# Kernel tuning notes

Hardware: AMD Instinct MI355X
Metric: run time of the kernel (lower is better)

Reference implementation:

```python
import jax, jax.numpy as jnp
import numpy as np

N = 4096
IN_DIM = 128
OUT_DIM = 64
LEAKY_SLOPE = 0.2


def setup_inputs() -> dict:
    key = jax.random.key(0)
    ks = jax.random.split(key, 8)
    H = jax.random.normal(ks[0], (N, IN_DIM), dtype=jnp.float32)
    # dense 0/1 adjacency per relation (int constants w.r.t. autodiff)
    A_buys = jax.random.randint(ks[1], (N, N), 0, 2, dtype=jnp.int32)
    A_views = jax.random.randint(ks[2], (N, N), 0, 2, dtype=jnp.int32)
    # xavier_uniform for W (stored [in, out]; Wh = H @ W == torch Linear with weight W.T)
    s_w = float(np.sqrt(6.0 / (IN_DIM + OUT_DIM)))
    W_buys = jax.random.uniform(ks[3], (IN_DIM, OUT_DIM), jnp.float32, -s_w, s_w)
    W_views = jax.random.uniform(ks[4], (IN_DIM, OUT_DIM), jnp.float32, -s_w, s_w)
    # xavier_uniform on a.view(1, 2*out_dim)
    s_a = float(np.sqrt(6.0 / (1 + 2 * OUT_DIM)))
    a_buys = jax.random.uniform(ks[5], (2 * OUT_DIM,), jnp.float32, -s_a, s_a)
    a_views = jax.random.uniform(ks[6], (2 * OUT_DIM,), jnp.float32, -s_a, s_a)
    bias = jnp.zeros((OUT_DIM,), dtype=jnp.float32)
    return {"H": H, "A_buys": A_buys, "A_views": A_views,
            "W_buys": W_buys, "W_views": W_views,
            "a_buys": a_buys, "a_views": a_views, "bias": bias}


def _relation(H, A, W, a):
    Wh = H @ W                                  # [N, OUT]
    # (cat(Wh_i, Wh_j) * a).sum(-1) == Wh_i @ a[:OUT] + Wh_j @ a[OUT:]
    s_i = Wh @ a[:OUT_DIM]                      # [N]
    s_j = Wh @ a[OUT_DIM:]                      # [N]
    e = jax.nn.leaky_relu(s_i[:, None] + s_j[None, :], LEAKY_SLOPE)  # [N, N]
    e = jnp.where(A == 0, -jnp.inf, e)
    alpha = jnp.nan_to_num(jax.nn.softmax(e, axis=1))                # isolated rows -> 0
    return alpha @ Wh                           # [N, OUT]


def reference(H, A_buys, A_views, W_buys, W_views, a_buys, a_views, bias):
    agg = _relation(H, A_buys, W_buys, a_buys) + _relation(H, A_views, W_views, a_views)
    return agg + bias
```

## Files before the change

kernel.cpp:

```cpp
#include <hip/hip_runtime.h>

#define NN 4096
#define IND 128
#define OUTD 64
#define NSPLIT 2

typedef __attribute__((ext_vector_type(4))) float  floatx4;
typedef __attribute__((ext_vector_type(8))) __bf16 bf16x8;
typedef __attribute__((ext_vector_type(4))) int    intx4;

__device__ __forceinline__ unsigned short f2bf(float f) {
  unsigned int u = __float_as_uint(f);
  u += 0x7fffu + ((u >> 16) & 1u);
  return (unsigned short)(u >> 16);
}

__device__ __forceinline__ float wcalc(int a, float s) {
  float l = s > 0.f ? s : 0.2f * s;
  float e = __expf(l);
  return a != 0 ? e : 0.f;
}

__global__ __launch_bounds__(256) void gat_prep(
    const float* __restrict__ H,
    const float* __restrict__ W0, const float* __restrict__ W1,
    const float* __restrict__ av0, const float* __restrict__ av1,
    unsigned short* __restrict__ whT,
    float* __restrict__ sA,
    float* __restrict__ sB)
{
  const int rel = blockIdx.y;
  const float* __restrict__ W  = rel ? W1 : W0;
  const float* __restrict__ av = rel ? av1 : av0;
  const int i0 = blockIdx.x * 16;
  const int t = threadIdx.x;
  const int c = t & 63;
  const int wv = __builtin_amdgcn_readfirstlane(t >> 6);
  const float* __restrict__ hp = H + (size_t)(i0 + wv * 4) * IND;

  float acc0 = 0.f, acc1 = 0.f, acc2 = 0.f, acc3 = 0.f;
#pragma unroll 8
  for (int k = 0; k < IND; k += 4) {
    float4 h0 = *(const float4*)(hp + k);
    float4 h1 = *(const float4*)(hp + IND + k);
    float4 h2 = *(const float4*)(hp + 2 * IND + k);
    float4 h3 = *(const float4*)(hp + 3 * IND + k);
    float w0 = W[(k + 0) * OUTD + c];
    float w1 = W[(k + 1) * OUTD + c];
    float w2 = W[(k + 2) * OUTD + c];
    float w3 = W[(k + 3) * OUTD + c];
    acc0 += h0.x * w0 + h0.y * w1 + h0.z * w2 + h0.w * w3;
    acc1 += h1.x * w0 + h1.y * w1 + h1.z * w2 + h1.w * w3;
    acc2 += h2.x * w0 + h2.y * w1 + h2.z * w2 + h2.w * w3;
    acc3 += h3.x * w0 + h3.y * w1 + h3.z * w2 + h3.w * w3;
  }

  const float alo = av[c], ahi = av[OUTD + c];
  float pa0 = acc0 * alo, pa1 = acc1 * alo, pa2 = acc2 * alo, pa3 = acc3 * alo;
  float pb0 = acc0 * ahi, pb1 = acc1 * ahi, pb2 = acc2 * ahi, pb3 = acc3 * ahi;
#pragma unroll
  for (int off = 32; off >= 1; off >>= 1) {
    pa0 += __shfl_xor(pa0, off); pa1 += __shfl_xor(pa1, off);
    pa2 += __shfl_xor(pa2, off); pa3 += __shfl_xor(pa3, off);
    pb0 += __shfl_xor(pb0, off); pb1 += __shfl_xor(pb1, off);
    pb2 += __shfl_xor(pb2, off); pb3 += __shfl_xor(pb3, off);
  }
  const int ibase = i0 + wv * 4;
  if (c == 0) {
    float* sa = sA + rel * NN + ibase;
    float* sb = sB + rel * NN + ibase;
    sa[0] = pa0; sa[1] = pa1; sa[2] = pa2; sa[3] = pa3;
    sb[0] = pb0; sb[1] = pb1; sb[2] = pb2; sb[3] = pb3;
  }

  unsigned long long packed =
      (unsigned long long)f2bf(acc0)        | ((unsigned long long)f2bf(acc1) << 16) |
      ((unsigned long long)f2bf(acc2) << 32) | ((unsigned long long)f2bf(acc3) << 48);
  *(unsigned long long*)(whT + (size_t)(rel * OUTD + c) * NN + ibase) = packed;
}

__global__ __launch_bounds__(512) void gat_main(
    const int* __restrict__ A0, const int* __restrict__ A1,
    const unsigned short* __restrict__ whT,
    const float* __restrict__ sA, const float* __restrict__ sB,
    float* __restrict__ numer,
    float* __restrict__ denom)
{
  __shared__ float red[8][1024];
  __shared__ float dred[8][16];
  const int rel  = blockIdx.y;
  const int sp   = blockIdx.z;
  const int i0   = blockIdx.x * 16;
  const int t    = threadIdx.x;
  const int w    = t >> 6;
  const int lane = t & 63;
  const int m    = lane & 15;
  const int quad = lane >> 4;
  const int i    = i0 + m;
  const int* __restrict__ A = rel ? A1 : A0;
  const float si = sA[rel * NN + i];
  const float* __restrict__ sb = sB + rel * NN;
  const unsigned short* __restrict__ wh = whT + (size_t)rel * OUTD * NN;

  const int jbase = sp * (NN / NSPLIT) + w * 256 + quad * 8;
  const int*            pA  = A  + (size_t)i * NN + jbase;
  const float*          psb = sb + jbase;
  const unsigned short* pb0 = wh + (size_t)(0 * 16 + m) * NN + jbase;
  const unsigned short* pb1 = wh + (size_t)(1 * 16 + m) * NN + jbase;
  const unsigned short* pb2 = wh + (size_t)(2 * 16 + m) * NN + jbase;
  const unsigned short* pb3 = wh + (size_t)(3 * 16 + m) * NN + jbase;

  floatx4 acc0 = {0.f, 0.f, 0.f, 0.f}, acc1 = acc0, acc2 = acc0, acc3 = acc0;
  float dsum = 0.f;

#pragma unroll 2
  for (int jt = 0; jt < 256; jt += 32) {
    intx4 a0 = __builtin_nontemporal_load((const intx4*)(pA + jt));
    intx4 a1 = __builtin_nontemporal_load((const intx4*)(pA + jt + 4));
    float4 s0 = *(const float4*)(psb + jt);
    float4 s1 = *(const float4*)(psb + jt + 4);
    bf16x8 b0 = *(const bf16x8*)(pb0 + jt);
    bf16x8 b1 = *(const bf16x8*)(pb1 + jt);
    bf16x8 b2 = *(const bf16x8*)(pb2 + jt);
    bf16x8 b3 = *(const bf16x8*)(pb3 + jt);

    float e0 = wcalc(a0[0], si + s0.x);
    float e1 = wcalc(a0[1], si + s0.y);
    float e2 = wcalc(a0[2], si + s0.z);
    float e3 = wcalc(a0[3], si + s0.w);
    float e4 = wcalc(a1[0], si + s1.x);
    float e5 = wcalc(a1[1], si + s1.y);
    float e6 = wcalc(a1[2], si + s1.z);
    float e7 = wcalc(a1[3], si + s1.w);
    dsum += ((e0 + e1) + (e2 + e3)) + ((e4 + e5) + (e6 + e7));

    bf16x8 af;
    af[0] = (__bf16)e0; af[1] = (__bf16)e1; af[2] = (__bf16)e2; af[3] = (__bf16)e3;
    af[4] = (__bf16)e4; af[5] = (__bf16)e5; af[6] = (__bf16)e6; af[7] = (__bf16)e7;

    acc0 = __builtin_amdgcn_mfma_f32_16x16x32_bf16(af, b0, acc0, 0, 0, 0);
    acc1 = __builtin_amdgcn_mfma_f32_16x16x32_bf16(af, b1, acc1, 0, 0, 0);
    acc2 = __builtin_amdgcn_mfma_f32_16x16x32_bf16(af, b2, acc2, 0, 0, 0);
    acc3 = __builtin_amdgcn_mfma_f32_16x16x32_bf16(af, b3, acc3, 0, 0, 0);
  }

  dsum += __shfl_xor(dsum, 16);
  dsum += __shfl_xor(dsum, 32);

#pragma unroll
  for (int r = 0; r < 4; r++) {
    const int row = quad * 4 + r;
    red[w][row * 64 + 0 * 16 + m] = acc0[r];
    red[w][row * 64 + 1 * 16 + m] = acc1[r];
    red[w][row * 64 + 2 * 16 + m] = acc2[r];
    red[w][row * 64 + 3 * 16 + m] = acc3[r];
  }
  if (lane < 16) dred[w][lane] = dsum;
  __syncthreads();

  const int c  = t & 63;
  const int r0 = t >> 6;
  const size_t base = ((size_t)rel * NSPLIT + sp) * NN;
#pragma unroll
  for (int rr = r0; rr < 16; rr += 8) {
    float ns = 0.f, ds = 0.f;
#pragma unroll
    for (int ww = 0; ww < 8; ww++) { ns += red[ww][rr * 64 + c]; ds += dred[ww][rr]; }
    numer[(base + i0 + rr) * OUTD + c] = ns;
    if (c == 0) denom[base + i0 + rr] = ds;
  }
}

__global__ __launch_bounds__(256) void gat_combine(
    const float* __restrict__ numer, const float* __restrict__ denom,
    const float* __restrict__ bias, float* __restrict__ out)
{
  const int idx = blockIdx.x * 256 + threadIdx.x;
  const int i  = idx >> 4;
  const int c4 = idx & 15;
  const float4* nv = (const float4*)numer;

  float4 o = ((const float4*)bias)[c4];
#pragma unroll
  for (int rel = 0; rel < 2; rel++) {
    float4 n = {0.f, 0.f, 0.f, 0.f};
    float  d = 0.f;
#pragma unroll
    for (int s = 0; s < NSPLIT; s++) {
      const size_t base = ((size_t)rel * NSPLIT + s) * NN + i;
      float4 np = nv[base * 16 + c4];
      n.x += np.x; n.y += np.y; n.z += np.z; n.w += np.w;
      d += denom[base];
    }
    float inv = d > 0.f ? 1.f / d : 0.f;
    o.x += n.x * inv; o.y += n.y * inv; o.z += n.z * inv; o.w += n.w * inv;
  }
  ((float4*)out)[idx] = o;
}

extern "C" void kernel_launch(void* const* d_in, const int* in_sizes, int n_in,
                              void* d_out, int out_size, void* d_ws, size_t ws_size,
                              hipStream_t stream) {
  const float* H    = (const float*)d_in[0];
  const int*   A0   = (const int*)d_in[1];
  const int*   A1   = (const int*)d_in[2];
  const float* W0   = (const float*)d_in[3];
  const float* W1   = (const float*)d_in[4];
  const float* av0  = (const float*)d_in[5];
  const float* av1  = (const float*)d_in[6];
  const float* bias = (const float*)d_in[7];
  float* out = (float*)d_out;

  unsigned short* whT = (unsigned short*)d_ws;
  float* sA    = (float*)((char*)d_ws + 2u * OUTD * NN * 2u);
  float* sB    = sA + 2 * NN;
  float* numer = sB + 2 * NN;
  float* denom = numer + (size_t)2 * NSPLIT * NN * OUTD;

  gat_prep<<<dim3(NN / 16, 2), 256, 0, stream>>>(H, W0, W1, av0, av1, whT, sA, sB);
  gat_main<<<dim3(NN / 16, 2, NSPLIT), 512, 0, stream>>>(A0, A1, whT, sA, sB, numer, denom);
  gat_combine<<<(NN * OUTD / 4) / 256, 256, 0, stream>>>(numer, denom, bias, out);
}
```

Before: 209.3 us.

## Pack adjacency into bitmasks in a separate pass before the attention kernel

A new gat_pack kernel uses wave ballots to compress both int32 adjacency matrices into 64-bit bitmasks. The main kernel then reads those bits instead of int32 values, which cuts the adjacency traffic it has to stream. The exponent is folded to exp2 with log2(e) pre-multiplied into the attention vectors, and leaky-relu becomes an fmax. The split count is now chosen at runtime from the workspace size. The full int32 adjacency is still read once by the pack pass, which adds a kernel launch and a bitmask write/read round trip.

```diff
diff --git a/kernel.cpp b/kernel.cpp
--- a/kernel.cpp
+++ b/kernel.cpp
@@ -3,11 +3,17 @@
 #define NN 4096
 #define IND 128
 #define OUTD 64
-#define NSPLIT 2
+#define LOG2E 1.44269504088896340736f
 
 typedef __attribute__((ext_vector_type(4))) float  floatx4;
 typedef __attribute__((ext_vector_type(8))) __bf16 bf16x8;
-typedef __attribute__((ext_vector_type(4))) int    intx4;
+typedef __attribute__((ext_vector_type(2))) unsigned long long u64x2;
+
+#if __has_builtin(__builtin_amdgcn_exp2f)
+#define EXP2(x) __builtin_amdgcn_exp2f(x)
+#else
+#define EXP2(x) exp2f(x)
+#endif
 
 __device__ __forceinline__ unsigned short f2bf(float f) {
   unsigned int u = __float_as_uint(f);
@@ -15,10 +21,32 @@
   return (unsigned short)(u >> 16);
 }
 
-__device__ __forceinline__ float wcalc(int a, float s) {
-  float l = s > 0.f ? s : 0.2f * s;
-  float e = __expf(l);
-  return a != 0 ? e : 0.f;
+__global__ __launch_bounds__(256) void gat_pack(
+    const int* __restrict__ A0, const int* __restrict__ A1,
+    unsigned long long* __restrict__ bits)
+{
+  const int t    = threadIdx.x;
+  const int lane = t & 63;
+  const int wv   = t >> 6;
+  const int unit = blockIdx.x * 4 + wv;
+  const int q    = unit & 3;
+  const int i    = (unit >> 2) & (NN - 1);
+  const int rel  = unit >> 14;
+  const int* __restrict__ A = (rel ? A1 : A0) + (size_t)i * NN + q * 1024 + lane;
+
+  unsigned long long wbuf[16];
+#pragma unroll
+  for (int k = 0; k < 16; k++)
+    wbuf[k] = __ballot(A[k * 64] != 0);
+
+  if (lane == 0) {
+    u64x2* dst = (u64x2*)(bits + ((size_t)rel * NN + i) * 64 + q * 16);
+#pragma unroll
+    for (int k = 0; k < 8; k++) {
+      u64x2 v; v[0] = wbuf[2 * k]; v[1] = wbuf[2 * k + 1];
+      dst[k] = v;
+    }
+  }
 }
 
 __global__ __launch_bounds__(256) void gat_prep(
@@ -55,7 +83,7 @@
     acc3 += h3.x * w0 + h3.y * w1 + h3.z * w2 + h3.w * w3;
   }
 
-  const float alo = av[c], ahi = av[OUTD + c];
+  const float alo = av[c] * LOG2E, ahi = av[OUTD + c] * LOG2E;
   float pa0 = acc0 * alo, pa1 = acc1 * alo, pa2 = acc2 * alo, pa3 = acc3 * alo;
   float pb0 = acc0 * ahi, pb1 = acc1 * ahi, pb2 = acc2 * ahi, pb3 = acc3 * ahi;
 #pragma unroll
@@ -80,11 +108,12 @@
 }
 
 __global__ __launch_bounds__(512) void gat_main(
-    const int* __restrict__ A0, const int* __restrict__ A1,
+    const unsigned long long* __restrict__ bits,
     const unsigned short* __restrict__ whT,
     const float* __restrict__ sA, const float* __restrict__ sB,
     float* __restrict__ numer,
-    float* __restrict__ denom)
+    float* __restrict__ denom,
+    int ns)
 {
   __shared__ float red[8][1024];
   __shared__ float dred[8][16];
@@ -97,51 +126,70 @@
   const int m    = lane & 15;
   const int quad = lane >> 4;
   const int i    = i0 + m;
-  const int* __restrict__ A = rel ? A1 : A0;
   const float si = sA[rel * NN + i];
   const float* __restrict__ sb = sB + rel * NN;
   const unsigned short* __restrict__ wh = whT + (size_t)rel * OUTD * NN;
-
-  const int jbase = sp * (NN / NSPLIT) + w * 256 + quad * 8;
-  const int*            pA  = A  + (size_t)i * NN + jbase;
-  const float*          psb = sb + jbase;
-  const unsigned short* pb0 = wh + (size_t)(0 * 16 + m) * NN + jbase;
-  const unsigned short* pb1 = wh + (size_t)(1 * 16 + m) * NN + jbase;
-  const unsigned short* pb2 = wh + (size_t)(2 * 16 + m) * NN + jbase;
-  const unsigned short* pb3 = wh + (size_t)(3 * 16 + m) * NN + jbase;
+  const unsigned long long* __restrict__ bp = bits + ((size_t)rel * NN + i) * 64;
+
+  const int jwin = NN / (ns * 8);
+  const int jw0  = sp * (NN / ns) + w * jwin;
+  const int nch  = jwin >> 8;
 
   floatx4 acc0 = {0.f, 0.f, 0.f, 0.f}, acc1 = acc0, acc2 = acc0, acc3 = acc0;
   float dsum = 0.f;
 
-#pragma unroll 2
-  for (int jt = 0; jt < 256; jt += 32) {
-    intx4 a0 = __builtin_nontemporal_load((const intx4*)(pA + jt));
-    intx4 a1 = __builtin_nontemporal_load((const intx4*)(pA + jt + 4));
-    float4 s0 = *(const float4*)(psb + jt);
-    float4 s1 = *(const float4*)(psb + jt + 4);
-    bf16x8 b0 = *(const bf16x8*)(pb0 + jt);
-    bf16x8 b1 = *(const bf16x8*)(pb1 + jt);
-    bf16x8 b2 = *(const bf16x8*)(pb2 + jt);
-    bf16x8 b3 = *(const bf16x8*)(pb3 + jt);
-
-    float e0 = wcalc(a0[0], si + s0.x);
-    float e1 = wcalc(a0[1], si + s0.y);
-    float e2 = wcalc(a0[2], si + s0.z);
-    float e3 = wcalc(a0[3], si + s0.w);
-    float e4 = wcalc(a1[0], si + s1.x);
-    float e5 = wcalc(a1[1], si + s1.y);
-    float e6 = wcalc(a1[2], si + s1.z);
-    float e7 = wcalc(a1[3], si + s1.w);
-    dsum += ((e0 + e1) + (e2 + e3)) + ((e4 + e5) + (e6 + e7));
-
-    bf16x8 af;
-    af[0] = (__bf16)e0; af[1] = (__bf16)e1; af[2] = (__bf16)e2; af[3] = (__bf16)e3;
-    af[4] = (__bf16)e4; af[5] = (__bf16)e5; af[6] = (__bf16)e6; af[7] = (__bf16)e7;
-
-    acc0 = __builtin_amdgcn_mfma_f32_16x16x32_bf16(af, b0, acc0, 0, 0, 0);
-    acc1 = __builtin_amdgcn_mfma_f32_16x16x32_bf16(af, b1, acc1, 0, 0, 0);
-    acc2 = __builtin_amdgcn_mfma_f32_16x16x32_bf16(af, b2, acc2, 0, 0, 0);
-    acc3 = __builtin_amdgcn_mfma_f32_16x16x32_bf16(af, b3, acc3, 0, 0, 0);
+  for (int c2 = 0; c2 < nch; c2++) {
+    const int jc = jw0 + c2 * 256;
+    u64x2 bA = *(const u64x2*)(bp + (jc >> 6));
+    u64x2 bB = *(const u64x2*)(bp + (jc >> 6) + 2);
+    const float*          psb = sb + jc + quad * 8;
+    const unsigned short* pb0 = wh + (size_t)(0 * 16 + m) * NN + jc + quad * 8;
+    const unsigned short* pb1 = wh + (size_t)(1 * 16 + m) * NN + jc + quad * 8;
+    const unsigned short* pb2 = wh + (size_t)(2 * 16 + m) * NN + jc + quad * 8;
+    const unsigned short* pb3 = wh + (size_t)(3 * 16 + m) * NN + jc + quad * 8;
+
+#pragma unroll
+    for (int jt = 0; jt < 256; jt += 32) {
+      float4 s0 = *(const float4*)(psb + jt);
+      float4 s1 = *(const float4*)(psb + jt + 4);
+      bf16x8 b0 = *(const bf16x8*)(pb0 + jt);
+      bf16x8 b1 = *(const bf16x8*)(pb1 + jt);
+      bf16x8 b2 = *(const bf16x8*)(pb2 + jt);
+      bf16x8 b3 = *(const bf16x8*)(pb3 + jt);
+
+      const unsigned long long wbits =
+          (jt < 64) ? bA[0] : (jt < 128) ? bA[1] : (jt < 192) ? bB[0] : bB[1];
+      const unsigned bmask = (unsigned)(wbits >> ((jt & 63) + quad * 8)) & 0xFFu;
+
+      float t0 = si + s0.x, t1 = si + s0.y, t2 = si + s0.z, t3 = si + s0.w;
+      float t4 = si + s1.x, t5 = si + s1.y, t6 = si + s1.z, t7 = si + s1.w;
+      float e0 = EXP2(fmaxf(t0, 0.2f * t0));
+      float e1 = EXP2(fmaxf(t1, 0.2f * t1));
+      float e2 = EXP2(fmaxf(t2, 0.2f * t2));
+      float e3 = EXP2(fmaxf(t3, 0.2f * t3));
+      float e4 = EXP2(fmaxf(t4, 0.2f * t4));
+      float e5 = EXP2(fmaxf(t5, 0.2f * t5));
+      float e6 = EXP2(fmaxf(t6, 0.2f * t6));
+      float e7 = EXP2(fmaxf(t7, 0.2f * t7));
+      e0 = (bmask & 1u)   ? e0 : 0.f;
+      e1 = (bmask & 2u)   ? e1 : 0.f;
+      e2 = (bmask & 4u)   ? e2 : 0.f;
+      e3 = (bmask & 8u)   ? e3 : 0.f;
+      e4 = (bmask & 16u)  ? e4 : 0.f;
+      e5 = (bmask & 32u)  ? e5 : 0.f;
+      e6 = (bmask & 64u)  ? e6 : 0.f;
+      e7 = (bmask & 128u) ? e7 : 0.f;
+      dsum += ((e0 + e1) + (e2 + e3)) + ((e4 + e5) + (e6 + e7));
+
+      bf16x8 af;
+      af[0] = (__bf16)e0; af[1] = (__bf16)e1; af[2] = (__bf16)e2; af[3] = (__bf16)e3;
+      af[4] = (__bf16)e4; af[5] = (__bf16)e5; af[6] = (__bf16)e6; af[7] = (__bf16)e7;
+
+      acc0 = __builtin_amdgcn_mfma_f32_16x16x32_bf16(af, b0, acc0, 0, 0, 0);
+      acc1 = __builtin_amdgcn_mfma_f32_16x16x32_bf16(af, b1, acc1, 0, 0, 0);
+      acc2 = __builtin_amdgcn_mfma_f32_16x16x32_bf16(af, b2, acc2, 0, 0, 0);
+      acc3 = __builtin_amdgcn_mfma_f32_16x16x32_bf16(af, b3, acc3, 0, 0, 0);
+    }
   }
 
   dsum += __shfl_xor(dsum, 16);
@@ -160,20 +208,20 @@
 
   const int c  = t & 63;
   const int r0 = t >> 6;
-  const size_t base = ((size_t)rel * NSPLIT + sp) * NN;
+  const size_t base = ((size_t)rel * ns + sp) * NN;
 #pragma unroll
   for (int rr = r0; rr < 16; rr += 8) {
-    float ns = 0.f, ds = 0.f;
-#pragma unroll
-    for (int ww = 0; ww < 8; ww++) { ns += red[ww][rr * 64 + c]; ds += dred[ww][rr]; }
-    numer[(base + i0 + rr) * OUTD + c] = ns;
+    float nsum = 0.f, ds = 0.f;
+#pragma unroll
+    for (int ww = 0; ww < 8; ww++) { nsum += red[ww][rr * 64 + c]; ds += dred[ww][rr]; }
+    numer[(base + i0 + rr) * OUTD + c] = nsum;
     if (c == 0) denom[base + i0 + rr] = ds;
   }
 }
 
 __global__ __launch_bounds__(256) void gat_combine(
     const float* __restrict__ numer, const float* __restrict__ denom,
-    const float* __restrict__ bias, float* __restrict__ out)
+    const float* __restrict__ bias, float* __restrict__ out, int ns)
 {
   const int idx = blockIdx.x * 256 + threadIdx.x;
   const int i  = idx >> 4;
@@ -185,9 +233,8 @@
   for (int rel = 0; rel < 2; rel++) {
     float4 n = {0.f, 0.f, 0.f, 0.f};
     float  d = 0.f;
-#pragma unroll
-    for (int s = 0; s < NSPLIT; s++) {
-      const size_t base = ((size_t)rel * NSPLIT + s) * NN + i;
+    for (int s = 0; s < ns; s++) {
+      const size_t base = ((size_t)rel * ns + s) * NN + i;
       float4 np = nv[base * 16 + c4];
       n.x += np.x; n.y += np.y; n.z += np.z; n.w += np.w;
       d += denom[base];
@@ -211,13 +258,21 @@
   const float* bias = (const float*)d_in[7];
   float* out = (float*)d_out;
 
-  unsigned short* whT = (unsigned short*)d_ws;
-  float* sA    = (float*)((char*)d_ws + 2u * OUTD * NN * 2u);
-  float* sB    = sA + 2 * NN;
-  float* numer = sB + 2 * NN;
-  float* denom = numer + (size_t)2 * NSPLIT * NN * OUTD;
-
+  const size_t whT_b = (size_t)2 * OUTD * NN * 2;
+  const size_t s_b   = (size_t)2 * NN * 4;
+  const size_t bit_b = (size_t)2 * NN * 64 * 8;
+  const size_t need2 = whT_b + 2 * s_b + bit_b + (size_t)2 * 2 * NN * OUTD * 4 + (size_t)2 * 2 * NN * 4;
+  const int ns = (ws_size >= need2) ? 2 : 1;
+
+  unsigned short*     whT  = (unsigned short*)d_ws;
+  float*              sA   = (float*)((char*)d_ws + whT_b);
+  float*              sB   = (float*)((char*)d_ws + whT_b + s_b);
+  unsigned long long* bits = (unsigned long long*)((char*)d_ws + whT_b + 2 * s_b);
+  float*              numer = (float*)((char*)d_ws + whT_b + 2 * s_b + bit_b);
+  float*              denom = numer + (size_t)2 * ns * NN * OUTD;
+
+  gat_pack<<<8192, 256, 0, stream>>>(A0, A1, bits);
   gat_prep<<<dim3(NN / 16, 2), 256, 0, stream>>>(H, W0, W1, av0, av1, whT, sA, sB);
-  gat_main<<<dim3(NN / 16, 2, NSPLIT), 512, 0, stream>>>(A0, A1, whT, sA, sB, numer, denom);
-  gat_combine<<<(NN * OUTD / 4) / 256, 256, 0, stream>>>(numer, denom, bias, out);
-}
+  gat_main<<<dim3(NN / 16, 2, ns), 512, 0, stream>>>(bits, whT, sA, sB, numer, denom, ns);
+  gat_combine<<<(NN * OUTD / 4) / 256, 256, 0, stream>>>(numer, denom, bias, out, ns);
+}
```

Result: slower. 214.0 us (+2.2%).
